# Kernel optimization log

Hardware: AMD Instinct MI355X
Metric: run time of the kernel (lower is better)

## Reference

```python
import jax, jax.numpy as jnp
import numpy as np

VOCAB, EMB, HID, SEQ, BATCH, LAYERS = 10000, 512, 1024, 128, 64, 2

def setup_inputs() -> dict:
    key = jax.random.key(0)
    ks = jax.random.split(key, 9)
    k_emb = np.sqrt(1.0 / HID)
    u = lambda k, shape, a: jax.random.uniform(k, shape, jnp.float32, -a, a)
    return {
        "inputs": jax.random.randint(ks[0], (SEQ, BATCH), 0, VOCAB),
        "hidden": jnp.zeros((LAYERS, BATCH, HID), jnp.float32),
        "emb": u(ks[1], (VOCAB, EMB), 0.1),
        "Wx0": u(ks[2], (HID, EMB), k_emb),
        "Wh0": u(ks[3], (HID, HID), k_emb),
        "bh0": u(ks[4], (HID,), k_emb),
        "Wx1": u(ks[5], (HID, HID), k_emb),
        "Wh1": u(ks[6], (HID, HID), k_emb),
        "bh1": u(ks[7], (HID,), k_emb),
        "Wout": u(ks[8], (VOCAB, HID), 0.1),
        "bout": u(jax.random.fold_in(key, 99), (VOCAB,), 0.1),
    }

def reference(inputs, hidden, emb, Wx0, Wh0, bh0, Wx1, Wh1, bh1, Wout, bout):
    # inputs: (S, B) int; hidden: (L, B, H). Dropout is identity (dp_keep_prob=1).
    embd = emb[inputs]  # (S, B, E)

    def step(h, x_t):
        h0 = jnp.tanh(x_t @ Wx0.T + h[0] @ Wh0.T + bh0)   # (B, H)
        h1 = jnp.tanh(h0 @ Wx1.T + h[1] @ Wh1.T + bh1)    # (B, H)
        logits_t = h1 @ Wout.T + bout                      # (B, V)
        return jnp.stack([h0, h1]), logits_t

    hidden_final, logits = jax.lax.scan(step, hidden, embd)
    return logits, hidden_final
```

## Files before the change

### kernel.cpp

```cpp
#include <hip/hip_runtime.h>
#include <hip/hip_bf16.h>


typedef unsigned short u16;
typedef unsigned int   u32;
typedef unsigned long long u64;
typedef __bf16 bf16x8 __attribute__((ext_vector_type(8)));
typedef float  f32x4  __attribute__((ext_vector_type(4)));

__device__ __forceinline__ u16 f2b(float f) {
  __hip_bfloat16 h = __float2bfloat16(f);
  return __builtin_bit_cast(u16, h);
}
__device__ __forceinline__ float b2f(u16 u) {
  return __bfloat162float(__builtin_bit_cast(__hip_bfloat16, u));
}

__device__ __forceinline__ void gload16(const void* g, void* lds) {
  __builtin_amdgcn_global_load_lds(
      (const __attribute__((address_space(1))) u32*)g,
      (__attribute__((address_space(3))) u32*)lds, 16, 0, 0);
}

__device__ __forceinline__ u64 aload64(const u64* p) {
  return __hip_atomic_load(p, __ATOMIC_RELAXED, __HIP_MEMORY_SCOPE_AGENT);
}
__device__ __forceinline__ void astore64(u64* p, u64 v) {
  __hip_atomic_store(p, v, __ATOMIC_RELAXED, __HIP_MEMORY_SCOPE_AGENT);
}
__device__ __forceinline__ int aloadi(const int* p) {
  return __hip_atomic_load(p, __ATOMIC_RELAXED, __HIP_MEMORY_SCOPE_AGENT);
}
__device__ __forceinline__ void astorei(int* p, int v) {
  __hip_atomic_store(p, v, __ATOMIC_RELAXED, __HIP_MEMORY_SCOPE_AGENT);
}
__device__ __forceinline__ int afetchadd(int* p) {
  return __hip_atomic_fetch_add(p, 1, __ATOMIC_RELAXED,
                                __HIP_MEMORY_SCOPE_AGENT);
}

__device__ __forceinline__ void stage16_512(char* hbuf, const u64* src,
                                            int tid) {
  const int rsub = tid >> 8;
  const int coff = tid & 255;
#pragma unroll
  for (int half = 0; half < 2; ++half) {
    u64 tmp[4];
#pragma unroll
    for (int i = 0; i < 4; ++i) {
      int it = half * 8 + i * 2 + rsub;
      tmp[i] = aload64(src + it * 256 + coff);
    }
#pragma unroll
    for (int i = 0; i < 4; ++i) {
      int it = half * 8 + i * 2 + rsub;
      *(u64*)(hbuf + it * 2048 + ((coff * 8) ^ ((it & 7) << 4))) = tmp[i];
    }
  }
}

__device__ __forceinline__ void cvt4(const float* __restrict__ s,
                                     u16* __restrict__ d, int n4,
                                     int gid, int stride) {
  for (int i = gid; i < n4; i += stride) {
    float4 f = ((const float4*)s)[i];
    ushort4 u;
    u.x = f2b(f.x); u.y = f2b(f.y); u.z = f2b(f.z); u.w = f2b(f.w);
    ((ushort4*)d)[i] = u;
  }
}

__global__ __launch_bounds__(256) void prep_kernel(
    const int* __restrict__ inputs, const float* __restrict__ hidden,
    const float* __restrict__ emb,
    const float* __restrict__ Wx0, const float* __restrict__ Wh0,
    const float* __restrict__ Wx1, const float* __restrict__ Wh1,
    const float* __restrict__ Wout,
    u16* Wx0b, u16* Wh0b, u16* Wcat1, u16* Woutb,
    u16* A0b, u16* Hh0, u16* Hh1, int* flags) {
  int gid = blockIdx.x * 256 + threadIdx.x;
  int stride = gridDim.x * 256;
  if (gid < 1024) flags[gid] = 0;
  cvt4(Wx0, Wx0b, 1024 * 512 / 4, gid, stride);
  cvt4(Wh0, Wh0b, 1024 * 1024 / 4, gid, stride);
  cvt4(Wout, Woutb, 10000 * 1024 / 4, gid, stride);
  cvt4(hidden, Hh0, 65536 / 4, gid, stride);
  cvt4(hidden + 65536, Hh1, 65536 / 4, gid, stride);
  for (int i = gid; i < 1024 * 512; i += stride) {
    int row = i >> 9, j = i & 511;
    float4 f = (j < 256) ? ((const float4*)Wx1)[row * 256 + j]
                         : ((const float4*)Wh1)[row * 256 + (j - 256)];
    ushort4 u;
    u.x = f2b(f.x); u.y = f2b(f.y); u.z = f2b(f.z); u.w = f2b(f.w);
    ((ushort4*)Wcat1)[i] = u;
  }
  for (int i = gid; i < 8192 * 128; i += stride) {
    int m = i >> 7, e4 = i & 127;
    int r = inputs[m];
    float4 f = ((const float4*)(emb + (size_t)r * 512))[e4];
    ushort4 u;
    u.x = f2b(f.x); u.y = f2b(f.y); u.z = f2b(f.z); u.w = f2b(f.w);
    ((ushort4*)A0b)[i] = u;
  }
}

__global__ __launch_bounds__(256) void gemm_bt(
    const u16* __restrict__ A, const u16* __restrict__ Bm,
    const float* __restrict__ bias, u16* __restrict__ Cout,
    int M, int N, int K) {
  const int tid = threadIdx.x;
  const int l = tid & 63;
  const int wv = tid >> 6;
  const int MT = M >> 7;
  const int bm = (int)blockIdx.x % MT;
  const int bn = (int)blockIdx.x / MT;
  const int m0 = bm * 128, n0 = bn * 128;

  __shared__ u16 As[128 * 32];
  __shared__ u16 Bs[128 * 32];

  const int fa0 = wv * 1024 + l * 16;
  const int fa1 = (4 + wv) * 1024 + l * 16;
  const int rowA0 = fa0 >> 6, kO0 = (fa0 & 63) >> 1;
  const int rowA1 = fa1 >> 6, kO1 = (fa1 & 63) >> 1;
  const u16* gA0 = A + (size_t)(m0 + rowA0) * K + kO0;
  const u16* gA1 = A + (size_t)(m0 + rowA1) * K + kO1;
  const u16* gB0 = Bm + (size_t)(n0 + rowA0) * K + kO0;
  const u16* gB1 = Bm + (size_t)(n0 + rowA1) * K + kO1;
  u16* lA0 = As + wv * 512;
  u16* lA1 = As + (4 + wv) * 512;
  u16* lB0 = Bs + wv * 512;
  u16* lB1 = Bs + (4 + wv) * 512;

  const int wm = wv >> 1, wn = wv & 1;
  const u16* pA = As + (wm * 64 + (l & 15)) * 32 + (l >> 4) * 8;
  const u16* pB = Bs + (wn * 64 + (l & 15)) * 32 + (l >> 4) * 8;

  f32x4 acc[4][4] = {};

  for (int k0 = 0; k0 < K; k0 += 32) {
    __syncthreads();
    gload16(gA0 + k0, lA0);
    gload16(gA1 + k0, lA1);
    gload16(gB0 + k0, lB0);
    gload16(gB1 + k0, lB1);
    asm volatile("s_waitcnt vmcnt(0)" ::: "memory");
    __syncthreads();
    bf16x8 a[4], b[4];
#pragma unroll
    for (int i = 0; i < 4; ++i) a[i] = *(const bf16x8*)(pA + i * 512);
#pragma unroll
    for (int j = 0; j < 4; ++j) b[j] = *(const bf16x8*)(pB + j * 512);
#pragma unroll
    for (int i = 0; i < 4; ++i)
#pragma unroll
      for (int j = 0; j < 4; ++j)
        acc[i][j] = __builtin_amdgcn_mfma_f32_16x16x32_bf16(a[i], b[j],
                                                            acc[i][j], 0, 0, 0);
  }

#pragma unroll
  for (int j = 0; j < 4; ++j) {
    int cn = n0 + wn * 64 + j * 16 + (l & 15);
    float bv = bias[cn];
#pragma unroll
    for (int i = 0; i < 4; ++i) {
      int rmb = m0 + wm * 64 + i * 16 + ((l >> 4) << 2);
#pragma unroll
      for (int r = 0; r < 4; ++r)
        Cout[(size_t)(rmb + r) * N + cn] = f2b(acc[i][j][r] + bv);
    }
  }
}

__global__ __launch_bounds__(512, 2) void rnn_fused(
    const u16* __restrict__ X0, const u16* __restrict__ Wh0b,
    const u16* __restrict__ Wcat1, const float* __restrict__ bh1,
    u16* __restrict__ Hh0, u16* __restrict__ Hh1,
    const u16* __restrict__ Woutb, const float* __restrict__ bout,
    float* __restrict__ outL,
    float* __restrict__ hfin0, float* __restrict__ hfin1,
    int* __restrict__ flags) {
  __shared__ __align__(16) char smem[40960];
  const int tid = threadIdx.x;
  const int l = tid & 63;
  const int wv = tid >> 6;

  if (blockIdx.x < 64) {
    char* hbuf = smem;
    float (*red)[16][16] = (float(*)[16][16])(smem + 32768);
    u16* ht = (u16*)(smem + 38912);
    const int wg = (int)blockIdx.x;
    const int bg = wg & 3, cc = wg >> 2;
    const int cw = wv & 3, kw = wv >> 2;
    const int col = cc * 64 + cw * 16 + (l & 15);
    const int row = l & 15;
    const int sw = (row & 7) << 4;
    const int rowoff = row * 2048;
    const int kwbase = kw * 1024 + ((l >> 4) << 4);
    bf16x8 b[16];
    {
      const u16* wp = Wh0b + (size_t)col * 1024 + (kw * 512 + ((l >> 4) * 8));
#pragma unroll
      for (int kt = 0; kt < 16; ++kt) b[kt] = *(const bf16x8*)(wp + kt * 32);
    }
    int* cnt0 = flags + (bg << 4);
    int* done0 = flags + 64 + (bg << 4);

    for (int t = 0; t < 128; ++t) {
      float xv[4];
      if (kw == 0) {
#pragma unroll
        for (int r = 0; r < 4; ++r) {
          int bat = bg * 16 + (l >> 4) * 4 + r;
          xv[r] = b2f(X0[(size_t)(t * 64 + bat) * 1024 + col]);
        }
      }
      stage16_512(hbuf, (const u64*)(Hh0 + ((size_t)t * 64 + bg * 16) * 1024),
                  tid);
      __syncthreads();
      f32x4 acc = {0.f, 0.f, 0.f, 0.f};
#pragma unroll
      for (int kt = 0; kt < 16; ++kt) {
        bf16x8 av =
            *(const bf16x8*)(hbuf + rowoff + ((kwbase + kt * 64) ^ sw));
        acc = __builtin_amdgcn_mfma_f32_16x16x32_bf16(av, b[kt], acc, 0, 0, 0);
      }
      if (kw == 1) {
#pragma unroll
        for (int r = 0; r < 4; ++r) red[cw][(l >> 4) * 4 + r][l & 15] = acc[r];
      }
      __syncthreads();
      if (kw == 0) {
#pragma unroll
        for (int r = 0; r < 4; ++r) {
          int br = (l >> 4) * 4 + r;
          float v = acc[r] + red[cw][br][l & 15] + xv[r];
          v = tanhf(v);
          ht[br * 64 + cw * 16 + (l & 15)] = f2b(v);
          if (t == 127) hfin0[(bg * 16 + br) * 1024 + col] = v;
        }
      }
      __syncthreads();
      if (tid < 256) {
        int rw = tid >> 4, seg = tid & 15;
        u64 v = ((const u64*)ht)[tid];
        u64* dp = (u64*)(Hh0 + ((size_t)(t + 1) * 64 + bg * 16 + rw) * 1024 +
                         cc * 64) + seg;
        astore64(dp, v);
      }
      asm volatile("s_waitcnt vmcnt(0)" ::: "memory");
      __syncthreads();
      if (tid == 0) {
        int old = afetchadd(cnt0);
        if (old == (t + 1) * 16 - 1) {
          astorei(done0, t + 1);
        } else if (t < 127) {
          while (aloadi(done0) < t + 1) __builtin_amdgcn_s_sleep(1);
        }
      }
      __syncthreads();
    }
  } else if (blockIdx.x < 192) {
    char* hbuf = smem;
    float (*red)[3][16][16] = (float(*)[3][16][16])(smem + 32768);
    u16* ht = (u16*)(smem + 38912);
    const int wg = (int)blockIdx.x - 64;
    const int bg = wg & 3, cc = wg >> 2;
    const int ch = wv & 1, kw = wv >> 1;
    const int col = cc * 32 + ch * 16 + (l & 15);
    const int row = l & 15;
    const int sw = (row & 7) << 4;
    const int rowoff = row * 2048;
    const int kwb = (kw & 1) * 1024 + ((l >> 4) << 4);
    bf16x8 b[16];
    {
      const u16* wp = Wcat1 + (size_t)col * 2048 + (kw * 512 + ((l >> 4) * 8));
#pragma unroll
      for (int kt = 0; kt < 16; ++kt) b[kt] = *(const bf16x8*)(wp + kt * 32);
    }
    const float bias = bh1[col];
    int* done0 = flags + 64 + (bg << 4);
    int* cnt1 = flags + 128 + (bg << 4);
    int* done1 = flags + 256 + (bg << 4);
    int* dlog = flags + 448 + (bg << 4);

    for (int s = 0; s < 128; ++s) {
      if (tid == 0) {
        while (aloadi(done0) < s + 1) __builtin_amdgcn_s_sleep(1);
      }
      __syncthreads();
      stage16_512(hbuf,
                  (const u64*)(Hh0 + ((size_t)(s + 1) * 64 + bg * 16) * 1024),
                  tid);
      __syncthreads();
      f32x4 acc = {0.f, 0.f, 0.f, 0.f};
      if (kw < 2) {
#pragma unroll
        for (int kt = 0; kt < 16; ++kt) {
          bf16x8 av = *(const bf16x8*)(hbuf + rowoff + ((kwb + kt * 64) ^ sw));
          acc =
              __builtin_amdgcn_mfma_f32_16x16x32_bf16(av, b[kt], acc, 0, 0, 0);
        }
      }
      __syncthreads();
      if (tid == 0) {
        while (aloadi(done1) < s) __builtin_amdgcn_s_sleep(1);
      }
      __syncthreads();
      stage16_512(hbuf, (const u64*)(Hh1 + ((size_t)s * 64 + bg * 16) * 1024),
                  tid);
      __syncthreads();
      if (kw >= 2) {
#pragma unroll
        for (int kt = 0; kt < 16; ++kt) {
          bf16x8 av = *(const bf16x8*)(hbuf + rowoff + ((kwb + kt * 64) ^ sw));
          acc =
              __builtin_amdgcn_mfma_f32_16x16x32_bf16(av, b[kt], acc, 0, 0, 0);
        }
      }
      if (kw != 0) {
#pragma unroll
        for (int r = 0; r < 4; ++r)
          red[ch][kw - 1][(l >> 4) * 4 + r][l & 15] = acc[r];
      }
      __syncthreads();
      if (kw == 0) {
#pragma unroll
        for (int r = 0; r < 4; ++r) {
          int br = (l >> 4) * 4 + r;
          int c = l & 15;
          float v = acc[r] + red[ch][0][br][c] + red[ch][1][br][c] +
                    red[ch][2][br][c] + bias;
          v = tanhf(v);
          ht[br * 32 + ch * 16 + c] = f2b(v);
          if (s == 127) hfin1[(bg * 16 + br) * 1024 + col] = v;
        }
      }
      __syncthreads();
      if (tid < 128) {
        int rw = tid >> 3, seg = tid & 7;
        u64 v = ((const u64*)ht)[tid];
        u64* dp = (u64*)(Hh1 + ((size_t)(s + 1) * 64 + bg * 16 + rw) * 1024 +
                         cc * 32) + seg;
        astore64(dp, v);
      }
      asm volatile("s_waitcnt vmcnt(0)" ::: "memory");
      __syncthreads();
      if (tid == 0) {
        int old = afetchadd(cnt1);
        if (old == (s + 1) * 32 - 1) {
          astorei(done1, s + 1);
          astorei(dlog, s + 1);
        }
      }
    }
  } else {
    const int sub = wv >> 2;
    const int wvl = wv & 3;
    u16* As = (u16*)(smem + sub * 16384);
    u16* Bs = (u16*)(smem + sub * 16384 + 8192);
    int* shid = (int*)(smem + 32768);
    int* workq = flags + 384;
    int* dlg = flags + 448;

    const int fa0 = wvl * 1024 + l * 16;
    const int fa1 = (4 + wvl) * 1024 + l * 16;
    const int rowA0 = fa0 >> 6, kO0 = (fa0 & 63) >> 1;
    const int rowA1 = fa1 >> 6, kO1 = (fa1 & 63) >> 1;
    const u16* Abase = Hh1 + 65536;
    u16* lB0 = Bs + wvl * 512;
    u16* lB1 = Bs + (4 + wvl) * 512;
    u64* dA0 = (u64*)((char*)As + wvl * 1024 + l * 16);
    u64* dA1 = (u64*)((char*)As + (4 + wvl) * 1024 + l * 16);
    const int wm = wvl >> 1, wn = wvl & 1;
    const u16* pA = As + (wm * 64 + (l & 15)) * 32 + (l >> 4) * 8;
    const u16* pB = Bs + (wn * 64 + (l & 15)) * 32 + (l >> 4) * 8;

    for (;;) {
      if (tid == 0) *shid = afetchadd(workq);
      __syncthreads();
      const int base = *shid;
      __syncthreads();
      if (base >= 2528) break;
      const int id = base * 2 + sub;
      const int u = id / 79, nn = id - u * 79;
      const int m0 = u * 128, n0 = nn * 128;

      if (tid == 0) {
        const int uhi = (base * 2 + 1) / 79;
        const int tgt = 2 * uhi + 2;
        for (;;) {
          int ok = 1;
#pragma unroll
          for (int g = 0; g < 4; ++g) ok &= (aloadi(dlg + g * 16) >= tgt);
          if (ok) break;
          __builtin_amdgcn_s_sleep(32);
        }
      }
      __syncthreads();

      const u16* gA0 = Abase + (size_t)(m0 + rowA0) * 1024 + kO0;
      const u16* gA1 = Abase + (size_t)(m0 + rowA1) * 1024 + kO1;
      int rB0 = n0 + rowA0; if (rB0 >= 10000) rB0 = 9999;
      int rB1 = n0 + rowA1; if (rB1 >= 10000) rB1 = 9999;
      const u16* gB0 = Woutb + (size_t)rB0 * 1024 + kO0;
      const u16* gB1 = Woutb + (size_t)rB1 * 1024 + kO1;

      f32x4 acc[4][4] = {};
      for (int k0 = 0; k0 < 1024; k0 += 32) {
        __syncthreads();
        const u64* pa0 = (const u64*)(gA0 + k0);
        const u64* pa1 = (const u64*)(gA1 + k0);
        u64 a00 = aload64(pa0), a01 = aload64(pa0 + 1);
        u64 a10 = aload64(pa1), a11 = aload64(pa1 + 1);
        gload16(gB0 + k0, lB0);
        gload16(gB1 + k0, lB1);
        dA0[0] = a00; dA0[1] = a01;
        dA1[0] = a10; dA1[1] = a11;
        asm volatile("s_waitcnt vmcnt(0)" ::: "memory");
        __syncthreads();
        bf16x8 a[4], b[4];
#pragma unroll
        for (int i = 0; i < 4; ++i) a[i] = *(const bf16x8*)(pA + i * 512);
#pragma unroll
        for (int j = 0; j < 4; ++j) b[j] = *(const bf16x8*)(pB + j * 512);
#pragma unroll
        for (int i = 0; i < 4; ++i)
#pragma unroll
          for (int j = 0; j < 4; ++j)
            acc[i][j] = __builtin_amdgcn_mfma_f32_16x16x32_bf16(
                a[i], b[j], acc[i][j], 0, 0, 0);
      }
#pragma unroll
      for (int j = 0; j < 4; ++j) {
        int cn = n0 + wn * 64 + j * 16 + (l & 15);
        if (cn >= 10000) continue;
        float bv = bout[cn];
#pragma unroll
        for (int i = 0; i < 4; ++i) {
          int rmb = m0 + wm * 64 + i * 16 + ((l >> 4) << 2);
#pragma unroll
          for (int r = 0; r < 4; ++r)
            outL[(size_t)(rmb + r) * 10000 + cn] = acc[i][j][r] + bv;
        }
      }
    }
  }
}

extern "C" void kernel_launch(void* const* d_in, const int* in_sizes, int n_in,
                              void* d_out, int out_size, void* d_ws,
                              size_t ws_size, hipStream_t stream) {
  const int*   inputs = (const int*)d_in[0];
  const float* hidden = (const float*)d_in[1];
  const float* emb    = (const float*)d_in[2];
  const float* Wx0    = (const float*)d_in[3];
  const float* Wh0    = (const float*)d_in[4];
  const float* bh0    = (const float*)d_in[5];
  const float* Wx1    = (const float*)d_in[6];
  const float* Wh1    = (const float*)d_in[7];
  const float* bh1    = (const float*)d_in[8];
  const float* Wout   = (const float*)d_in[9];
  const float* bout   = (const float*)d_in[10];
  float* out = (float*)d_out;

  if (ws_size < (size_t)88 * 1024 * 1024) return;

  char* w = (char*)d_ws;
  u16* Wx0b  = (u16*)w; w += 1048576;
  u16* Wh0b  = (u16*)w; w += 2097152;
  u16* Wcat1 = (u16*)w; w += 4194304;
  u16* Woutb = (u16*)w; w += 20480000;
  u16* A0b   = (u16*)w; w += 8388608;
  u16* X0b   = (u16*)w; w += 16777216;
  u16* Hh0   = (u16*)w; w += 16908288;
  u16* Hh1   = (u16*)w; w += 16908288;
  int* flags = (int*)w;

  float* hfin0 = out + 81920000;
  float* hfin1 = out + 81920000 + 65536;

  prep_kernel<<<2048, 256, 0, stream>>>(inputs, hidden, emb, Wx0, Wh0, Wx1,
                                        Wh1, Wout, Wx0b, Wh0b, Wcat1, Woutb,
                                        A0b, Hh0, Hh1, flags);
  gemm_bt<<<512, 256, 0, stream>>>(A0b, Wx0b, bh0, X0b, 8192, 1024, 512);
  rnn_fused<<<512, 512, 0, stream>>>(X0b, Wh0b, Wcat1, bh1, Hh0, Hh1, Woutb,
                                     bout, out, hfin0, hfin1, flags);
}
```

Before: 828.1 us.

## Double block size to 1024 threads, halve recurrent blocks, class-partitioned logits queue

```diff
diff --git a/kernel.cpp b/kernel.cpp
--- a/kernel.cpp
+++ b/kernel.cpp
@@ -39,23 +39,20 @@
                                 __HIP_MEMORY_SCOPE_AGENT);
 }
 
-__device__ __forceinline__ void stage16_512(char* hbuf, const u64* src,
-                                            int tid) {
+__device__ __forceinline__ void stage16_1024(char* hbuf, const u64* src,
+                                             int tid) {
   const int rsub = tid >> 8;
   const int coff = tid & 255;
-#pragma unroll
-  for (int half = 0; half < 2; ++half) {
-    u64 tmp[4];
-#pragma unroll
-    for (int i = 0; i < 4; ++i) {
-      int it = half * 8 + i * 2 + rsub;
-      tmp[i] = aload64(src + it * 256 + coff);
-    }
-#pragma unroll
-    for (int i = 0; i < 4; ++i) {
-      int it = half * 8 + i * 2 + rsub;
-      *(u64*)(hbuf + it * 2048 + ((coff * 8) ^ ((it & 7) << 4))) = tmp[i];
-    }
+  u64 tmp[4];
+#pragma unroll
+  for (int i = 0; i < 4; ++i) {
+    int it = i * 4 + rsub;
+    tmp[i] = aload64(src + it * 256 + coff);
+  }
+#pragma unroll
+  for (int i = 0; i < 4; ++i) {
+    int it = i * 4 + rsub;
+    *(u64*)(hbuf + it * 2048 + ((coff * 8) ^ ((it & 7) << 4))) = tmp[i];
   }
 }
 
@@ -173,7 +170,7 @@
   }
 }
 
-__global__ __launch_bounds__(512, 2) void rnn_fused(
+__global__ __launch_bounds__(1024, 4) void rnn_fused(
     const u16* __restrict__ X0, const u16* __restrict__ Wh0b,
     const u16* __restrict__ Wcat1, const float* __restrict__ bh1,
     u16* __restrict__ Hh0, u16* __restrict__ Hh1,
@@ -181,19 +178,19 @@
     float* __restrict__ outL,
     float* __restrict__ hfin0, float* __restrict__ hfin1,
     int* __restrict__ flags) {
-  __shared__ __align__(16) char smem[40960];
+  __shared__ __align__(16) char smem[65664];
   const int tid = threadIdx.x;
   const int l = tid & 63;
   const int wv = tid >> 6;
 
-  if (blockIdx.x < 64) {
+  if (blockIdx.x < 32) {
     char* hbuf = smem;
     float (*red)[16][16] = (float(*)[16][16])(smem + 32768);
-    u16* ht = (u16*)(smem + 38912);
+    u16* ht = (u16*)(smem + 40960);
     const int wg = (int)blockIdx.x;
     const int bg = wg & 3, cc = wg >> 2;
-    const int cw = wv & 3, kw = wv >> 2;
-    const int col = cc * 64 + cw * 16 + (l & 15);
+    const int cw = wv & 7, kw = wv >> 3;
+    const int col = cc * 128 + cw * 16 + (l & 15);
     const int row = l & 15;
     const int sw = (row & 7) << 4;
     const int rowoff = row * 2048;
@@ -216,8 +213,8 @@
           xv[r] = b2f(X0[(size_t)(t * 64 + bat) * 1024 + col]);
         }
       }
-      stage16_512(hbuf, (const u64*)(Hh0 + ((size_t)t * 64 + bg * 16) * 1024),
-                  tid);
+      stage16_1024(hbuf, (const u64*)(Hh0 + ((size_t)t * 64 + bg * 16) * 1024),
+                   tid);
       __syncthreads();
       f32x4 acc = {0.f, 0.f, 0.f, 0.f};
 #pragma unroll
@@ -237,23 +234,23 @@
           int br = (l >> 4) * 4 + r;
           float v = acc[r] + red[cw][br][l & 15] + xv[r];
           v = tanhf(v);
-          ht[br * 64 + cw * 16 + (l & 15)] = f2b(v);
+          ht[br * 128 + cw * 16 + (l & 15)] = f2b(v);
           if (t == 127) hfin0[(bg * 16 + br) * 1024 + col] = v;
         }
       }
       __syncthreads();
-      if (tid < 256) {
-        int rw = tid >> 4, seg = tid & 15;
+      if (tid < 512) {
+        int rw = tid >> 5, seg = tid & 31;
         u64 v = ((const u64*)ht)[tid];
         u64* dp = (u64*)(Hh0 + ((size_t)(t + 1) * 64 + bg * 16 + rw) * 1024 +
-                         cc * 64) + seg;
+                         cc * 128) + seg;
         astore64(dp, v);
       }
       asm volatile("s_waitcnt vmcnt(0)" ::: "memory");
       __syncthreads();
       if (tid == 0) {
         int old = afetchadd(cnt0);
-        if (old == (t + 1) * 16 - 1) {
+        if (old == (t + 1) * 8 - 1) {
           astorei(done0, t + 1);
         } else if (t < 127) {
           while (aloadi(done0) < t + 1) __builtin_amdgcn_s_sleep(1);
@@ -261,14 +258,14 @@
       }
       __syncthreads();
     }
-  } else if (blockIdx.x < 192) {
+  } else if (blockIdx.x < 96) {
     char* hbuf = smem;
     float (*red)[3][16][16] = (float(*)[3][16][16])(smem + 32768);
-    u16* ht = (u16*)(smem + 38912);
-    const int wg = (int)blockIdx.x - 64;
+    u16* ht = (u16*)(smem + 45056);
+    const int wg = (int)blockIdx.x - 32;
     const int bg = wg & 3, cc = wg >> 2;
-    const int ch = wv & 1, kw = wv >> 1;
-    const int col = cc * 32 + ch * 16 + (l & 15);
+    const int ch = wv & 3, kw = wv >> 2;
+    const int col = cc * 64 + ch * 16 + (l & 15);
     const int row = l & 15;
     const int sw = (row & 7) << 4;
     const int rowoff = row * 2048;
@@ -290,9 +287,9 @@
         while (aloadi(done0) < s + 1) __builtin_amdgcn_s_sleep(1);
       }
       __syncthreads();
-      stage16_512(hbuf,
-                  (const u64*)(Hh0 + ((size_t)(s + 1) * 64 + bg * 16) * 1024),
-                  tid);
+      stage16_1024(hbuf,
+                   (const u64*)(Hh0 + ((size_t)(s + 1) * 64 + bg * 16) * 1024),
+                   tid);
       __syncthreads();
       f32x4 acc = {0.f, 0.f, 0.f, 0.f};
       if (kw < 2) {
@@ -308,8 +305,8 @@
         while (aloadi(done1) < s) __builtin_amdgcn_s_sleep(1);
       }
       __syncthreads();
-      stage16_512(hbuf, (const u64*)(Hh1 + ((size_t)s * 64 + bg * 16) * 1024),
-                  tid);
+      stage16_1024(hbuf, (const u64*)(Hh1 + ((size_t)s * 64 + bg * 16) * 1024),
+                   tid);
       __syncthreads();
       if (kw >= 2) {
 #pragma unroll
@@ -333,23 +330,23 @@
           float v = acc[r] + red[ch][0][br][c] + red[ch][1][br][c] +
                     red[ch][2][br][c] + bias;
           v = tanhf(v);
-          ht[br * 32 + ch * 16 + c] = f2b(v);
+          ht[br * 64 + ch * 16 + c] = f2b(v);
           if (s == 127) hfin1[(bg * 16 + br) * 1024 + col] = v;
         }
       }
       __syncthreads();
-      if (tid < 128) {
-        int rw = tid >> 3, seg = tid & 7;
+      if (tid < 256) {
+        int rw = tid >> 4, seg = tid & 15;
         u64 v = ((const u64*)ht)[tid];
         u64* dp = (u64*)(Hh1 + ((size_t)(s + 1) * 64 + bg * 16 + rw) * 1024 +
-                         cc * 32) + seg;
+                         cc * 64) + seg;
         astore64(dp, v);
       }
       asm volatile("s_waitcnt vmcnt(0)" ::: "memory");
       __syncthreads();
       if (tid == 0) {
         int old = afetchadd(cnt1);
-        if (old == (s + 1) * 32 - 1) {
+        if (old == (s + 1) * 16 - 1) {
           astorei(done1, s + 1);
           astorei(dlog, s + 1);
         }
@@ -360,8 +357,10 @@
     const int wvl = wv & 3;
     u16* As = (u16*)(smem + sub * 16384);
     u16* Bs = (u16*)(smem + sub * 16384 + 8192);
-    int* shid = (int*)(smem + 32768);
-    int* workq = flags + 384;
+    int* shid = (int*)(smem + 65600);
+    const int cls = ((int)blockIdx.x - 96) & 7;
+    const int sz = (79 - cls + 7) / 8;
+    int* classq = flags + 640 + (cls << 4);
     int* dlg = flags + 448;
 
     const int fa0 = wvl * 1024 + l * 16;
@@ -378,18 +377,19 @@
     const u16* pB = Bs + (wn * 64 + (l & 15)) * 32 + (l >> 4) * 8;
 
     for (;;) {
-      if (tid == 0) *shid = afetchadd(workq);
+      if (tid == 0) *shid = afetchadd(classq);
       __syncthreads();
       const int base = *shid;
       __syncthreads();
-      if (base >= 2528) break;
-      const int id = base * 2 + sub;
-      const int u = id / 79, nn = id - u * 79;
+      if (base >= 16 * sz) break;
+      const int id = base * 4 + sub;
+      const int u = id / sz, j = id - u * sz;
+      const int nn = cls + j * 8;
       const int m0 = u * 128, n0 = nn * 128;
 
       if (tid == 0) {
-        const int uhi = (base * 2 + 1) / 79;
-        const int tgt = 2 * uhi + 2;
+        const int umax = (base * 4 + 3) / sz;
+        const int tgt = 2 * umax + 2;
         for (;;) {
           int ok = 1;
 #pragma unroll
@@ -424,17 +424,17 @@
 #pragma unroll
         for (int i = 0; i < 4; ++i) a[i] = *(const bf16x8*)(pA + i * 512);
 #pragma unroll
-        for (int j = 0; j < 4; ++j) b[j] = *(const bf16x8*)(pB + j * 512);
+        for (int j2 = 0; j2 < 4; ++j2) b[j2] = *(const bf16x8*)(pB + j2 * 512);
 #pragma unroll
         for (int i = 0; i < 4; ++i)
 #pragma unroll
-          for (int j = 0; j < 4; ++j)
-            acc[i][j] = __builtin_amdgcn_mfma_f32_16x16x32_bf16(
-                a[i], b[j], acc[i][j], 0, 0, 0);
-      }
-#pragma unroll
-      for (int j = 0; j < 4; ++j) {
-        int cn = n0 + wn * 64 + j * 16 + (l & 15);
+          for (int j2 = 0; j2 < 4; ++j2)
+            acc[i][j2] = __builtin_amdgcn_mfma_f32_16x16x32_bf16(
+                a[i], b[j2], acc[i][j2], 0, 0, 0);
+      }
+#pragma unroll
+      for (int j2 = 0; j2 < 4; ++j2) {
+        int cn = n0 + wn * 64 + j2 * 16 + (l & 15);
         if (cn >= 10000) continue;
         float bv = bout[cn];
 #pragma unroll
@@ -442,7 +442,7 @@
           int rmb = m0 + wm * 64 + i * 16 + ((l >> 4) << 2);
 #pragma unroll
           for (int r = 0; r < 4; ++r)
-            outL[(size_t)(rmb + r) * 10000 + cn] = acc[i][j][r] + bv;
+            outL[(size_t)(rmb + r) * 10000 + cn] = acc[i][j2][r] + bv;
         }
       }
     }
@@ -485,6 +485,6 @@
                                         Wh1, Wout, Wx0b, Wh0b, Wcat1, Woutb,
                                         A0b, Hh0, Hh1, flags);
   gemm_bt<<<512, 256, 0, stream>>>(A0b, Wx0b, bh0, X0b, 8192, 1024, 512);
-  rnn_fused<<<512, 512, 0, stream>>>(X0b, Wh0b, Wcat1, bh1, Hh0, Hh1, Woutb,
-                                     bout, out, hfin0, hfin1, flags);
-}
+  rnn_fused<<<256, 1024, 0, stream>>>(X0b, Wh0b, Wcat1, bh1, Hh0, Hh1, Woutb,
+                                      bout, out, hfin0, hfin1, flags);
+}
```

New measurement: 669.0 us, median of 2. 1.24x faster.
